# Kernel tuning notes

Measured on AMD Instinct MI355X. Metric: run time of the kernel, lower is better.

Reference implementation:

```python
import jax, jax.numpy as jnp
import numpy as np

N0, N1, N2 = 32, 32, 32
BOX = np.array([[0.0, 1.0], [0.0, 1.0], [0.0, 1.0]], dtype=np.float32)
N_VERTS, N_FACES = 512, 1024
EPS = 1.19209e-07
SEPS = float(np.sqrt(EPS))  # ~3.45e-4, matches torch code


def _freq_axis(n, lo, hi):
    # xi_k = (2k - (n-1)) * pi / (hi - lo)
    s = np.pi / (hi - lo)
    k = jnp.arange(n, dtype=jnp.float32)
    return (2.0 * k - (n - 1)) * jnp.float32(s)


def setup_inputs() -> dict:
    key = jax.random.key(0)
    k1, k2 = jax.random.split(key)
    Verts = jax.random.normal(k1, (N_VERTS, 3), dtype=jnp.float32)
    # distinct vertex indices per face -> non-degenerate triangles (a.s.)
    base = jax.random.randint(k2, (N_FACES, 1), 0, N_VERTS)
    Faces = (base + jnp.arange(3)[None, :]) % N_VERTS
    box_size = jnp.asarray(BOX)
    xi0 = _freq_axis(N0, BOX[0, 0], BOX[0, 1])
    xi1 = _freq_axis(N1, BOX[1, 0], BOX[1, 1])
    xi2 = _freq_axis(N2, BOX[2, 0], BOX[2, 1])
    return {"Verts": Verts, "box_size": box_size, "xi0": xi0, "xi1": xi1,
            "xi2": xi2, "Faces": Faces}


def _expmj(x):
    # exp(-i x) for real x -> complex64
    return jnp.exp(-1j * x)


def _fourier(Verts, box_size, xi0, xi1, xi2, Faces):
    V = Verts - box_size[:, 0]                      # shift into box frame
    coords = V[Faces]                               # (F, 3, 3)
    cross = jnp.cross(coords[:, 1] - coords[:, 0], coords[:, 2] - coords[:, 0])
    trisar = 0.5 * jnp.linalg.norm(cross, axis=1)   # (F,)
    meshar = jnp.sum(trisar)
    trisar = trisar * (2.0 / meshar)

    G0, G1, G2 = jnp.meshgrid(xi0, xi1, xi2, indexing="ij")
    Xi = jnp.stack([G0.ravel(), G1.ravel(), G2.ravel()], axis=1)  # (G, 3)
    xiv = Xi @ V.T                                  # (G, nV)

    xia = xiv[:, Faces[:, 0]]                       # (G, F)
    xib = xiv[:, Faces[:, 1]]
    xic = xiv[:, Faces[:, 2]]
    xiab = xib - xia
    xibc = xic - xib
    xica = xia - xic

    aab, abc, aca = jnp.abs(xiab), jnp.abs(xibc), jnp.abs(xica)
    s2, s3, s4 = aab < SEPS, abc < SEPS, aca < SEPS      # strict, for C1
    c2, c3, c4 = aab <= SEPS, abc <= SEPS, aca <= SEPS   # non-strict, C2-C4
    R1 = (s2 & s3) | (s3 & s4) | (s4 & s2)
    R2 = c2 & ~R1
    R3 = c3 & ~R2 & ~R1
    R4 = c4 & ~R3 & ~R2 & ~R1
    R5 = ~(R1 | R2 | R3 | R4)

    # R1: all edges collapse in frequency space
    v1 = _expmj((xia + xib + xic) / 3.0) / 2.0

    def _pair_case(mask, x1, x2, x3):
        # (i*exp(-i m) + (exp(-i m) - exp(-i x3)) / d) / d,  m=(x1+x2)/2, d=m-x3
        m = (x1 + x2) * 0.5
        d = jnp.where(mask, m - x3, 1.0)  # safe denominator off-mask
        em = _expmj(m)
        return (1j * em + (em - _expmj(x3)) / d) / d

    v2 = _pair_case(R2, xia, xib, xic)
    v3 = _pair_case(R3, xib, xic, xia)
    v4 = _pair_case(R4, xic, xia, xib)

    da = jnp.where(R5, xiab * xica, 1.0)
    db = jnp.where(R5, xibc * xiab, 1.0)
    dc = jnp.where(R5, xica * xibc, 1.0)
    v5 = _expmj(xia) / da + _expmj(xib) / db + _expmj(xic) / dc

    res = jnp.where(R1, v1,
          jnp.where(R2, v2,
          jnp.where(R3, v3,
          jnp.where(R4, v4, v5))))                  # (G, F) complex64

    ft = res @ trisar.astype(res.dtype)             # (G,)
    return ft.reshape(G0.shape)                     # (N0, N1, N2)


def reference(Verts, box_size, xi0, xi1, xi2, Faces):
    return _fourier(Verts, box_size, xi0, xi1, xi2, Faces)
```

## Files before the change

### kernel.cpp

```cpp
#include <hip/hip_runtime.h>
#include <math.h>


namespace {
constexpr int kNpts = 32 * 32 * 32;
constexpr int kHalf = kNpts / 2;
constexpr int kNF = 1024;
constexpr int kThreads = 1024;
constexpr int kWaves = 16;
constexpr int kFPW = kNF / kWaves;
constexpr int kBlocks = kHalf / 64;
constexpr int kSlowCap = 1536;
}

__device__ __forceinline__ float fract32(float x) {
#if __has_builtin(__builtin_amdgcn_fractf)
    return __builtin_amdgcn_fractf(x);
#else
    return x - floorf(x);
#endif
}

__device__ __forceinline__ void pair_case_f64(double x1, double x2, double x3,
                                              double& vr, double& vi) {
    const double m = (x1 + x2) * 0.5;
    const double d = m - x3;
    double sm, cm, s3, c3;
    sincos(m, &sm, &cm);
    sincos(x3, &s3, &c3);
    vr = (sm + (cm - c3) / d) / d;
    vi = (cm + (s3 - sm) / d) / d;
}

__device__ __noinline__ void slow_exact(
        int f, int p, const float* __restrict__ verts,
        const float* __restrict__ box, const int* __restrict__ faces,
        const float* __restrict__ xi0, const float* __restrict__ xi1,
        const float* __restrict__ xi2, float& cr, float& ci) {
    const double SEPS = __builtin_sqrt(1.19209e-07);
    const double TWO_PI = 6.283185307179586;
    const double INV_TWO_PI = 0.15915494309189535;

    const int i2 = p & 31, i1 = (p >> 5) & 31, i0 = p >> 10;
    const double xxd = (double)xi0[i0] * INV_TWO_PI;
    const double xyd = (double)xi1[i1] * INV_TWO_PI;
    const double xzd = (double)xi2[i2] * INV_TWO_PI;
    const double lo0 = (double)box[0], lo1 = (double)box[2], lo2 = (double)box[4];
    const int ia = faces[3 * f + 0], ib = faces[3 * f + 1], ic = faces[3 * f + 2];
    const double ax = (double)verts[3 * ia + 0] - lo0, ay = (double)verts[3 * ia + 1] - lo1, az = (double)verts[3 * ia + 2] - lo2;
    const double bx = (double)verts[3 * ib + 0] - lo0, by = (double)verts[3 * ib + 1] - lo1, bz = (double)verts[3 * ib + 2] - lo2;
    const double cx = (double)verts[3 * ic + 0] - lo0, cy = (double)verts[3 * ic + 1] - lo1, cz = (double)verts[3 * ic + 2] - lo2;
    const float axf = (float)ax, ayf = (float)ay, azf = (float)az;
    const float bxf = (float)bx, byf = (float)by, bzf = (float)bz;
    const float cxf = (float)cx, cyf = (float)cy, czf = (float)cz;
    const float e1x = bxf - axf, e1y = byf - ayf, e1z = bzf - azf;
    const float e2x = cxf - axf, e2y = cyf - ayf, e2z = czf - azf;
    const float crx = e1y * e2z - e1z * e2y;
    const float cry = e1z * e2x - e1x * e2z;
    const float crz = e1x * e2y - e1y * e2x;
    const float areaf = 0.5f * sqrtf(crx * crx + cry * cry + crz * crz);
    const double rad = fma(xzd, az, fma(xyd, ay, xxd * ax));
    const double rbd = fma(xzd, bz, fma(xyd, by, xxd * bx));
    const double rcd = fma(xzd, cz, fma(xyd, cy, xxd * cx));
    const double xa = rad * TWO_PI, xb = rbd * TWO_PI, xc = rcd * TWO_PI;
    const double dAB = xb - xa, dBC = xc - xb, dCA = xa - xc;
    const double aab = fabs(dAB), abc = fabs(dBC), aca = fabs(dCA);
    const bool s2 = aab < SEPS, s3 = abc < SEPS, s4 = aca < SEPS;
    const bool c2 = aab <= SEPS, c3 = abc <= SEPS, c4 = aca <= SEPS;
    const bool R1 = (s2 && s3) || (s3 && s4) || (s4 && s2);
    const bool R2 = c2 && !R1;
    const bool R3b = c3 && !R2 && !R1;
    const bool R4 = c4 && !R3b && !R2 && !R1;
    double vr, vi;
    if (R1) {
        const double m = ((xa + xb) + xc) / 3.0;
        double sm, cm;
        sincos(m, &sm, &cm);
        vr = cm / 2.0;
        vi = -sm / 2.0;
    } else if (R2) {
        pair_case_f64(xa, xb, xc, vr, vi);
    } else if (R3b) {
        pair_case_f64(xb, xc, xa, vr, vi);
    } else if (R4) {
        pair_case_f64(xc, xa, xb, vr, vi);
    } else {
        double sa, ca, sb, cb, sc, cc;
        sincos(xa, &sa, &ca);
        sincos(xb, &sb, &cb);
        sincos(xc, &sc, &cc);
        const double da = dAB * dCA, db = dBC * dAB, dc = dCA * dBC;
        vr = (ca / da + cb / db) + cc / dc;
        vi = -((sa / da + sb / db) + sc / dc);
    }
    cr = areaf * (float)vr;
    ci = areaf * (float)vi;
}

__global__ __launch_bounds__(kThreads, 4) void fourier_all(
        const float* __restrict__ verts, const float* __restrict__ box,
        const int* __restrict__ faces, const float* __restrict__ xi0,
        const float* __restrict__ xi1, const float* __restrict__ xi2,
        float* __restrict__ out, int interleaved) {
    const float INV_TWO_PI_F = 0.15915494f;
    const float TAUP_REV2 = 2.5330296e-5f;

    __shared__ float4 rec[kNF][3];
    __shared__ float accR[kWaves][64];
    __shared__ float accI[kWaves][64];
    __shared__ unsigned slowList[kSlowCap];
    __shared__ unsigned slowCnt;
    __shared__ float wsum[kWaves];
    __shared__ float meshar_sh;

    const int t = threadIdx.x;
    const int l = t & 63;
    const int w = t >> 6;
    const int pb = blockIdx.x;

    if (t == 0) slowCnt = 0;

    {
        const int f = t;
        const float lo0 = box[0], lo1 = box[2], lo2 = box[4];
        const int ia = faces[3 * f + 0], ib = faces[3 * f + 1], ic = faces[3 * f + 2];
        const float ax = verts[3 * ia + 0] - lo0, ay = verts[3 * ia + 1] - lo1, az = verts[3 * ia + 2] - lo2;
        const float bx = verts[3 * ib + 0] - lo0, by = verts[3 * ib + 1] - lo1, bz = verts[3 * ib + 2] - lo2;
        const float cx = verts[3 * ic + 0] - lo0, cy = verts[3 * ic + 1] - lo1, cz = verts[3 * ic + 2] - lo2;
        const float e1x = bx - ax, e1y = by - ay, e1z = bz - az;
        const float e2x = cx - ax, e2y = cy - ay, e2z = cz - az;
        const float crx = e1y * e2z - e1z * e2y;
        const float cry = e1z * e2x - e1x * e2z;
        const float crz = e1x * e2y - e1y * e2x;
        const float area = 0.5f * sqrtf(crx * crx + cry * cry + crz * crz);
        rec[f][0] = make_float4(ax, ay, az, bx);
        rec[f][1] = make_float4(by, bz, cx, cy);
        rec[f][2] = make_float4(cz, area * 0.025330296f, 0.0f, 0.0f);
        float a = area;
        a += __shfl_down(a, 32, 64);
        a += __shfl_down(a, 16, 64);
        a += __shfl_down(a, 8, 64);
        a += __shfl_down(a, 4, 64);
        a += __shfl_down(a, 2, 64);
        a += __shfl_down(a, 1, 64);
        if (l == 0) wsum[w] = a;
    }
    __syncthreads();
    if (t == 0) {
        float s = wsum[0];
#pragma unroll
        for (int j = 1; j < kWaves; ++j) s += wsum[j];
        meshar_sh = s;
    }

    const int p = pb * 64 + l;
    const int i2 = p & 31, i1 = (p >> 5) & 31, i0 = p >> 10;
    const float xxr = xi0[i0] * INV_TWO_PI_F;
    const float xyr = xi1[i1] * INV_TWO_PI_F;
    const float xzr = xi2[i2] * INV_TWO_PI_F;

    float re = 0.0f, im = 0.0f;
    const int fbase = w * kFPW;

#pragma unroll 4
    for (int i = 0; i < kFPW; ++i) {
        const float4 q0 = rec[fbase + i][0];
        const float4 q1 = rec[fbase + i][1];
        const float4 q2 = rec[fbase + i][2];
        const float ra = fmaf(xzr, q0.z, fmaf(xyr, q0.y, xxr * q0.x));
        const float rb = fmaf(xzr, q1.y, fmaf(xyr, q1.x, xxr * q0.w));
        const float rc = fmaf(xzr, q2.x, fmaf(xyr, q1.w, xxr * q1.z));
        const float fdab = rb - ra, fdbc = rc - rb, fdca = ra - rc;
        const float d1 = fdab * fdca;
        const float d2 = fdbc * fdab;
        const float d3 = fdca * fdbc;
        const float mn = fminf(fminf(fabsf(d1), fabsf(d2)), fabsf(d3));
        if (mn > TAUP_REV2) {
            const float R3w = __builtin_amdgcn_rcpf(d1 * fdbc) * q2.y;
            const float r1 = fdbc * R3w, r2 = fdca * R3w, r3 = fdab * R3w;
            const float fa = fract32(ra);
            const float fb = fract32(rb);
            const float fc = fract32(rc);
            const float sa = __builtin_amdgcn_sinf(fa), ca = __builtin_amdgcn_cosf(fa);
            const float sb = __builtin_amdgcn_sinf(fb), cb = __builtin_amdgcn_cosf(fb);
            const float sc = __builtin_amdgcn_sinf(fc), cc = __builtin_amdgcn_cosf(fc);
            re = fmaf(cc, r3, fmaf(cb, r2, fmaf(ca, r1, re)));
            im = fmaf(-sc, r3, fmaf(-sb, r2, fmaf(-sa, r1, im)));
        } else {
            const unsigned pos = atomicAdd(&slowCnt, 1u);
            if (pos < (unsigned)kSlowCap) {
                slowList[pos] = ((unsigned)(fbase + i) << 6) | (unsigned)l;
            } else {
                float cr, ci;
                slow_exact(fbase + i, p, verts, box, faces, xi0, xi1, xi2, cr, ci);
                re += cr;
                im += ci;
            }
        }
    }

    accR[w][l] = re;
    accI[w][l] = im;
    __syncthreads();

    {
        unsigned n = slowCnt;
        if (n > (unsigned)kSlowCap) n = (unsigned)kSlowCap;
        for (unsigned j = (unsigned)t; j < n; j += (unsigned)kThreads) {
            const unsigned e = slowList[j];
            const int f = (int)(e >> 6);
            const int lane = (int)(e & 63u);
            float cr, ci;
            slow_exact(f, pb * 64 + lane, verts, box, faces, xi0, xi1, xi2, cr, ci);
            atomicAdd(&accR[0][lane], cr);
            atomicAdd(&accI[0][lane], ci);
        }
    }
    __syncthreads();

    if (t < 64) {
        float R = accR[0][l], I = accI[0][l];
#pragma unroll
        for (int g = 1; g < kWaves; ++g) { R += accR[g][l]; I += accI[g][l]; }
        const float inv2 = 2.0f / meshar_sh;
        R *= inv2;
        I *= inv2;
        const int q = kNpts - 1 - p;
        if (interleaved) {
            ((float2*)out)[p] = make_float2(R, I);
            ((float2*)out)[q] = make_float2(R, -I);
        } else {
            out[p] = R;
            out[q] = R;
        }
    }
}

extern "C" void kernel_launch(void* const* d_in, const int* in_sizes, int n_in,
                              void* d_out, int out_size, void* d_ws, size_t ws_size,
                              hipStream_t stream) {
    const float* verts = (const float*)d_in[0];
    const float* box   = (const float*)d_in[1];
    const float* xi0v  = (const float*)d_in[2];
    const float* xi1v  = (const float*)d_in[3];
    const float* xi2v  = (const float*)d_in[4];
    const int*   faces = (const int*)d_in[5];
    (void)d_ws; (void)ws_size;

    const int interleaved = (out_size == 2 * kNpts) ? 1 : 0;

    hipLaunchKernelGGL(fourier_all, dim3(kBlocks), dim3(kThreads), 0, stream,
                       verts, box, faces, xi0v, xi1v, xi2v,
                       (float*)d_out, interleaved);
}
```

Before: 90.60 us.

## Split faces across two blocks per point tile and accumulate with atomics

Each 64-point tile is now handled by two blocks, each covering half the faces. This doubles the grid from 256 to 512 blocks so more of the GPU's compute units are busy, and halves the shared-memory record table. The deferred slow-path list with its shared atomics is replaced by a per-thread bitmask whose slow faces are processed inline after the main loop. Outputs are combined with global float atomicAdd after a hipMemsetAsync zeroes them, which adds a memset and makes summation order nondeterministic.

```diff
diff --git a/kernel.cpp b/kernel.cpp
--- a/kernel.cpp
+++ b/kernel.cpp
@@ -8,9 +8,9 @@
 constexpr int kNF = 1024;
 constexpr int kThreads = 1024;
 constexpr int kWaves = 16;
-constexpr int kFPW = kNF / kWaves;
-constexpr int kBlocks = kHalf / 64;
-constexpr int kSlowCap = 1536;
+constexpr int kFaceHalves = 2;
+constexpr int kFPW = (kNF / kFaceHalves) / kWaves;
+constexpr int kBlocks = (kHalf / 64) * kFaceHalves;
 }
 
 __device__ __forceinline__ float fract32(float x) {
@@ -97,7 +97,7 @@
     ci = areaf * (float)vi;
 }
 
-__global__ __launch_bounds__(kThreads, 4) void fourier_all(
+__global__ __launch_bounds__(kThreads, 8) void fourier_all(
         const float* __restrict__ verts, const float* __restrict__ box,
         const int* __restrict__ faces, const float* __restrict__ xi0,
         const float* __restrict__ xi1, const float* __restrict__ xi2,
@@ -105,20 +105,17 @@
     const float INV_TWO_PI_F = 0.15915494f;
     const float TAUP_REV2 = 2.5330296e-5f;
 
-    __shared__ float4 rec[kNF][3];
+    __shared__ float4 rec[kNF / kFaceHalves][3];
     __shared__ float accR[kWaves][64];
     __shared__ float accI[kWaves][64];
-    __shared__ unsigned slowList[kSlowCap];
-    __shared__ unsigned slowCnt;
     __shared__ float wsum[kWaves];
     __shared__ float meshar_sh;
 
     const int t = threadIdx.x;
     const int l = t & 63;
     const int w = t >> 6;
-    const int pb = blockIdx.x;
-
-    if (t == 0) slowCnt = 0;
+    const int pb = blockIdx.x & 255;
+    const int fh = blockIdx.x >> 8;
 
     {
         const int f = t;
@@ -133,9 +130,12 @@
         const float cry = e1z * e2x - e1x * e2z;
         const float crz = e1x * e2y - e1y * e2x;
         const float area = 0.5f * sqrtf(crx * crx + cry * cry + crz * crz);
-        rec[f][0] = make_float4(ax, ay, az, bx);
-        rec[f][1] = make_float4(by, bz, cx, cy);
-        rec[f][2] = make_float4(cz, area * 0.025330296f, 0.0f, 0.0f);
+        if ((f >> 9) == fh) {
+            const int r = f & 511;
+            rec[r][0] = make_float4(ax, ay, az, bx);
+            rec[r][1] = make_float4(by, bz, cx, cy);
+            rec[r][2] = make_float4(cz, area * 0.025330296f, 0.0f, 0.0f);
+        }
         float a = area;
         a += __shfl_down(a, 32, 64);
         a += __shfl_down(a, 16, 64);
@@ -160,13 +160,14 @@
     const float xzr = xi2[i2] * INV_TWO_PI_F;
 
     float re = 0.0f, im = 0.0f;
-    const int fbase = w * kFPW;
+    unsigned slowMask = 0u;
+    const int rbase = w * kFPW;
 
 #pragma unroll 4
     for (int i = 0; i < kFPW; ++i) {
-        const float4 q0 = rec[fbase + i][0];
-        const float4 q1 = rec[fbase + i][1];
-        const float4 q2 = rec[fbase + i][2];
+        const float4 q0 = rec[rbase + i][0];
+        const float4 q1 = rec[rbase + i][1];
+        const float4 q2 = rec[rbase + i][2];
         const float ra = fmaf(xzr, q0.z, fmaf(xyr, q0.y, xxr * q0.x));
         const float rb = fmaf(xzr, q1.y, fmaf(xyr, q1.x, xxr * q0.w));
         const float rc = fmaf(xzr, q2.x, fmaf(xyr, q1.w, xxr * q1.z));
@@ -187,35 +188,25 @@
             re = fmaf(cc, r3, fmaf(cb, r2, fmaf(ca, r1, re)));
             im = fmaf(-sc, r3, fmaf(-sb, r2, fmaf(-sa, r1, im)));
         } else {
-            const unsigned pos = atomicAdd(&slowCnt, 1u);
-            if (pos < (unsigned)kSlowCap) {
-                slowList[pos] = ((unsigned)(fbase + i) << 6) | (unsigned)l;
-            } else {
-                float cr, ci;
-                slow_exact(fbase + i, p, verts, box, faces, xi0, xi1, xi2, cr, ci);
-                re += cr;
-                im += ci;
-            }
+            slowMask |= (1u << i);
         }
+    }
+
+    if (slowMask) {
+        const int gbase = fh * 512 + rbase;
+        unsigned m = slowMask;
+        do {
+            const int i = __builtin_ctz(m);
+            m &= m - 1u;
+            float cr, ci;
+            slow_exact(gbase + i, p, verts, box, faces, xi0, xi1, xi2, cr, ci);
+            re += cr;
+            im += ci;
+        } while (m);
     }
 
     accR[w][l] = re;
     accI[w][l] = im;
-    __syncthreads();
-
-    {
-        unsigned n = slowCnt;
-        if (n > (unsigned)kSlowCap) n = (unsigned)kSlowCap;
-        for (unsigned j = (unsigned)t; j < n; j += (unsigned)kThreads) {
-            const unsigned e = slowList[j];
-            const int f = (int)(e >> 6);
-            const int lane = (int)(e & 63u);
-            float cr, ci;
-            slow_exact(f, pb * 64 + lane, verts, box, faces, xi0, xi1, xi2, cr, ci);
-            atomicAdd(&accR[0][lane], cr);
-            atomicAdd(&accI[0][lane], ci);
-        }
-    }
     __syncthreads();
 
     if (t < 64) {
@@ -227,11 +218,13 @@
         I *= inv2;
         const int q = kNpts - 1 - p;
         if (interleaved) {
-            ((float2*)out)[p] = make_float2(R, I);
-            ((float2*)out)[q] = make_float2(R, -I);
+            atomicAdd(&out[2 * p + 0], R);
+            atomicAdd(&out[2 * p + 1], I);
+            atomicAdd(&out[2 * q + 0], R);
+            atomicAdd(&out[2 * q + 1], -I);
         } else {
-            out[p] = R;
-            out[q] = R;
+            atomicAdd(&out[p], R);
+            atomicAdd(&out[q], R);
         }
     }
 }
@@ -249,6 +242,7 @@
 
     const int interleaved = (out_size == 2 * kNpts) ? 1 : 0;
 
+    hipMemsetAsync(d_out, 0, (size_t)out_size * sizeof(float), stream);
     hipLaunchKernelGGL(fourier_all, dim3(kBlocks), dim3(kThreads), 0, stream,
                        verts, box, faces, xi0v, xi1v, xi2v,
                        (float*)d_out, interleaved);
```

Result: slower. 92.59 us (+2.2%).

## Replace shared slow-path work queue with per-thread bitmask and deferred in-thread evaluation

Applied to the files above, without the earlier changes.

Removes the block-wide shared-memory slow list, its atomic counter and the extra barrier phase that redistributed near-degenerate face/point pairs across all threads. Each thread now records its slow faces in a 64-bit mask and evaluates them itself after the fast loop. This avoids shared atomics and a __syncthreads, and frees shared memory that may help occupancy. The cost is wave divergence: the slow double-precision path is no longer load-balanced across the block, so a few lanes with many slow faces can stall their whole wave.

```diff
diff --git a/kernel.cpp b/kernel.cpp
--- a/kernel.cpp
+++ b/kernel.cpp
@@ -10,7 +10,6 @@
 constexpr int kWaves = 16;
 constexpr int kFPW = kNF / kWaves;
 constexpr int kBlocks = kHalf / 64;
-constexpr int kSlowCap = 1536;
 }
 
 __device__ __forceinline__ float fract32(float x) {
@@ -108,8 +107,6 @@
     __shared__ float4 rec[kNF][3];
     __shared__ float accR[kWaves][64];
     __shared__ float accI[kWaves][64];
-    __shared__ unsigned slowList[kSlowCap];
-    __shared__ unsigned slowCnt;
     __shared__ float wsum[kWaves];
     __shared__ float meshar_sh;
 
@@ -117,8 +114,6 @@
     const int l = t & 63;
     const int w = t >> 6;
     const int pb = blockIdx.x;
-
-    if (t == 0) slowCnt = 0;
 
     {
         const int f = t;
@@ -160,6 +155,7 @@
     const float xzr = xi2[i2] * INV_TWO_PI_F;
 
     float re = 0.0f, im = 0.0f;
+    unsigned long long slowMask = 0ull;
     const int fbase = w * kFPW;
 
 #pragma unroll 4
@@ -187,35 +183,24 @@
             re = fmaf(cc, r3, fmaf(cb, r2, fmaf(ca, r1, re)));
             im = fmaf(-sc, r3, fmaf(-sb, r2, fmaf(-sa, r1, im)));
         } else {
-            const unsigned pos = atomicAdd(&slowCnt, 1u);
-            if (pos < (unsigned)kSlowCap) {
-                slowList[pos] = ((unsigned)(fbase + i) << 6) | (unsigned)l;
-            } else {
-                float cr, ci;
-                slow_exact(fbase + i, p, verts, box, faces, xi0, xi1, xi2, cr, ci);
-                re += cr;
-                im += ci;
-            }
+            slowMask |= (1ull << i);
         }
+    }
+
+    if (slowMask) {
+        unsigned long long m = slowMask;
+        do {
+            const int i = (int)__builtin_ctzll(m);
+            m &= m - 1ull;
+            float cr, ci;
+            slow_exact(fbase + i, p, verts, box, faces, xi0, xi1, xi2, cr, ci);
+            re += cr;
+            im += ci;
+        } while (m);
     }
 
     accR[w][l] = re;
     accI[w][l] = im;
-    __syncthreads();
-
-    {
-        unsigned n = slowCnt;
-        if (n > (unsigned)kSlowCap) n = (unsigned)kSlowCap;
-        for (unsigned j = (unsigned)t; j < n; j += (unsigned)kThreads) {
-            const unsigned e = slowList[j];
-            const int f = (int)(e >> 6);
-            const int lane = (int)(e & 63u);
-            float cr, ci;
-            slow_exact(f, pb * 64 + lane, verts, box, faces, xi0, xi1, xi2, cr, ci);
-            atomicAdd(&accR[0][lane], cr);
-            atomicAdd(&accI[0][lane], ci);
-        }
-    }
     __syncthreads();
 
     if (t < 64) {
```

Measured after the change: 91.90 us. About the same (+1.4%).
